# Optimization experiments

Measured on AMD Instinct MI355X. Metric: run time of the kernel, lower is better.

The kernel has to match this reference:

```python
import jax, jax.numpy as jnp
import numpy as np


def setup_inputs() -> dict:
    key = jax.random.key(0)
    ks = jax.random.split(key, 6)
    B, T, U, D_in, D_inner, V = 4, 150, 40, 512, 512, 4000
    s = 1.0 / np.sqrt(D_in)
    return {
        "enc_state": jax.random.normal(ks[0], (B, T, D_in), jnp.float32),
        "dec_state": jax.random.normal(ks[1], (B, U, D_in), jnp.float32),
        "W_enc": jax.random.normal(ks[2], (D_inner, D_in), jnp.float32) * s,
        "b_enc": jnp.zeros((D_inner,), jnp.float32),
        "W_prd": jax.random.normal(ks[3], (D_inner, D_in), jnp.float32) * s,
        "b_prd": jnp.zeros((D_inner,), jnp.float32),
        "W_proj": jax.random.normal(ks[4], (V, D_inner), jnp.float32) * (1.0 / np.sqrt(D_inner)),
        "b_proj": jnp.zeros((V,), jnp.float32),
    }


def reference(enc_state, dec_state, W_enc, b_enc, W_prd, b_prd, W_proj, b_proj):
    # pre-linear projections: [B,T,Di] and [B,U,Di]
    enc = jnp.einsum("btd,id->bti", enc_state, W_enc) + b_enc
    dec = jnp.einsum("bud,id->bui", dec_state, W_prd) + b_prd
    # broadcast add -> [B,T,U,Di] (joint_func='add', post_linear=False)
    joint = jnp.tanh(enc[:, :, None, :] + dec[:, None, :, :])
    # project to vocab and log-softmax: [B,T,U,V]
    logits = jnp.einsum("btui,vi->btuv", joint, W_proj) + b_proj
    return jax.nn.log_softmax(logits, axis=-1)
```

## Files before the change

kernel.cpp:

```cpp
#include <hip/hip_runtime.h>
#include <stdint.h>

typedef unsigned short u16;
typedef __attribute__((ext_vector_type(8))) short short8;
typedef __attribute__((ext_vector_type(4))) float floatx4;

#define D_IN  512
#define M_TOT 24000
#define M_PAD 24064
#define V_DIM 4000
#define V_PAD 4096
#define T_DIM 150
#define U_DIM 40

__device__ __forceinline__ u16 f2bf(float f) {
    union { float f; uint32_t u; } v; v.f = f;
    uint32_t r = v.u + 0x7FFF + ((v.u >> 16) & 1);
    return (u16)(r >> 16);
}

__device__ __forceinline__ void gld_lds16(const u16* g, u16* l) {
    __builtin_amdgcn_global_load_lds(
        (const __attribute__((address_space(1))) void*)g,
        (__attribute__((address_space(3))) void*)l,
        16, 0, 0);
}

__global__ void k_pre(const float* __restrict__ enc_state, const float* __restrict__ dec_state,
                      const float* __restrict__ W_enc, const float* __restrict__ b_enc,
                      const float* __restrict__ W_prd, const float* __restrict__ b_prd,
                      float* __restrict__ enc_o, float* __restrict__ dec_o,
                      float* __restrict__ sumexp)
{
    int gid = (blockIdx.y * gridDim.x + blockIdx.x) * blockDim.x + threadIdx.x;
    if (gid < M_TOT) sumexp[gid] = 0.f;

    const float* Ag; const float* Wg; const float* bg; float* Og; int M;
    int by = blockIdx.y;
    if (by < 19) { Ag = enc_state; Wg = W_enc; bg = b_enc; Og = enc_o; M = 600; }
    else         { Ag = dec_state; Wg = W_prd; bg = b_prd; Og = dec_o; M = 160; by -= 19; }

    const int row0 = by * 32;
    const int col0 = blockIdx.x * 64;
    __shared__ float Ash[32][17];
    __shared__ float Bsh[64][17];
    const int tid = threadIdx.x;
    const int tr = tid & 31;
    const int tc = tid >> 5;
    float accv[8] = {0.f,0.f,0.f,0.f,0.f,0.f,0.f,0.f};

    for (int k0 = 0; k0 < D_IN; k0 += 16) {
        __syncthreads();
        #pragma unroll
        for (int s = 0; s < 2; ++s) {
            int idx = tid + s * 256;
            int r = idx >> 4, c = idx & 15;
            Ash[r][c] = (row0 + r < M) ? Ag[(size_t)(row0 + r) * D_IN + k0 + c] : 0.f;
        }
        #pragma unroll
        for (int s = 0; s < 4; ++s) {
            int idx = tid + s * 256;
            int r = idx >> 4, c = idx & 15;
            Bsh[r][c] = Wg[(size_t)(col0 + r) * D_IN + k0 + c];
        }
        __syncthreads();
        #pragma unroll
        for (int kk = 0; kk < 16; ++kk) {
            float a = Ash[tr][kk];
            #pragma unroll
            for (int j = 0; j < 8; ++j) accv[j] += a * Bsh[tc * 8 + j][kk];
        }
    }
    if (row0 + tr < M) {
        #pragma unroll
        for (int j = 0; j < 8; ++j)
            Og[(size_t)(row0 + tr) * D_IN + col0 + tc * 8 + j] = accv[j] + bg[col0 + tc * 8 + j];
    }
}

__global__ void k_wconv(const float* __restrict__ W_proj, u16* __restrict__ Wp)
{
    int gid = blockIdx.x * blockDim.x + threadIdx.x;
    int idx2 = gid * 2;
    if (idx2 >= V_PAD * D_IN) return;
    int row = idx2 >> 9;
    ushort2 w;
    if (row < V_DIM) {
        w.x = f2bf(W_proj[idx2]);
        w.y = f2bf(W_proj[idx2 + 1]);
    } else { w.x = 0; w.y = 0; }
    *(ushort2*)&Wp[idx2] = w;
}

__global__ void k_joint(const float* __restrict__ enc_o, const float* __restrict__ dec_o,
                        u16* __restrict__ J)
{
    int m = blockIdx.x;
    int i = threadIdx.x * 2;
    ushort2 w;
    if (m < M_TOT) {
        int b = m / (T_DIM * U_DIM);
        int r = m % (T_DIM * U_DIM);
        int t = r / U_DIM, u = r % U_DIM;
        const float* e = enc_o + (size_t)(b * T_DIM + t) * D_IN + i;
        const float* d = dec_o + (size_t)(b * U_DIM + u) * D_IN + i;
        w.x = f2bf(tanhf(e[0] + d[0]));
        w.y = f2bf(tanhf(e[1] + d[1]));
    } else { w.x = 0; w.y = 0; }
    *(ushort2*)&J[(size_t)m * D_IN + i] = w;
}

__global__ __launch_bounds__(256, 2) void k_gemm(const u16* __restrict__ A,
                                                 const u16* __restrict__ Bt,
                                                 const float* __restrict__ bias,
                                                 float* __restrict__ C,
                                                 float* __restrict__ sumexp)
{
    __shared__ u16 Ash[128 * 32];
    __shared__ u16 Bsh[128 * 32];
    const int row0 = blockIdx.x * 128;
    const int col0 = blockIdx.y * 128;
    const int tid  = threadIdx.x;
    const int wave = tid >> 6;
    const int lane = tid & 63;
    const int wm = wave >> 1, wn = wave & 1;
    const int lrow = lane & 15;
    const int lq   = lane >> 4;
    const int srow = lane >> 2;
    const int scol = (lane & 3) * 8;

    floatx4 acc[4][4] = {};

    for (int k0 = 0; k0 < D_IN; k0 += 32) {
        __syncthreads();
        #pragma unroll
        for (int s = 0; s < 2; ++s) {
            int c = wave * 2 + s;
            gld_lds16(A  + (size_t)(row0 + c * 16 + srow) * D_IN + k0 + scol, &Ash[c * 16 * 32]);
            gld_lds16(Bt + (size_t)(col0 + c * 16 + srow) * D_IN + k0 + scol, &Bsh[c * 16 * 32]);
        }
        __syncthreads();
        short8 af[4], bf[4];
        #pragma unroll
        for (int mi = 0; mi < 4; ++mi)
            af[mi] = *(const short8*)&Ash[(wm * 64 + mi * 16 + lrow) * 32 + lq * 8];
        #pragma unroll
        for (int nj = 0; nj < 4; ++nj)
            bf[nj] = *(const short8*)&Bsh[(wn * 64 + nj * 16 + lrow) * 32 + lq * 8];
        #pragma unroll
        for (int mi = 0; mi < 4; ++mi)
            #pragma unroll
            for (int nj = 0; nj < 4; ++nj)
                acc[mi][nj] = __builtin_amdgcn_mfma_f32_16x16x32_bf16(af[mi], bf[nj], acc[mi][nj], 0, 0, 0);
    }

    const int cbase = col0 + wn * 64;
    const int rbase = row0 + wm * 64;
    float bv[4];
    #pragma unroll
    for (int nj = 0; nj < 4; ++nj) {
        int cc = cbase + nj * 16 + lrow;
        bv[nj] = (cc < V_DIM) ? bias[cc] : 0.f;
    }
    #pragma unroll
    for (int mi = 0; mi < 4; ++mi) {
        float se[4] = {0.f, 0.f, 0.f, 0.f};
        #pragma unroll
        for (int nj = 0; nj < 4; ++nj) {
            int cc = cbase + nj * 16 + lrow;
            bool cok = (cc < V_DIM);
            #pragma unroll
            for (int r = 0; r < 4; ++r) {
                float logit = acc[mi][nj][r] + bv[nj];
                int rr = rbase + mi * 16 + lq * 4 + r;
                if (cok) {
                    if (rr < M_TOT) C[(size_t)rr * V_DIM + cc] = logit;
                    se[r] += __expf(logit);
                }
            }
        }
        #pragma unroll
        for (int msk = 1; msk < 16; msk <<= 1) {
            #pragma unroll
            for (int r = 0; r < 4; ++r) se[r] += __shfl_xor(se[r], msk, 64);
        }
        if (lrow == 0) {
            #pragma unroll
            for (int r = 0; r < 4; ++r) {
                int rr = rbase + mi * 16 + lq * 4 + r;
                if (rr < M_TOT) atomicAdd(&sumexp[rr], se[r]);
            }
        }
    }
}

__global__ void k_lse(float* __restrict__ C, const float* __restrict__ sumexp)
{
    int gid = blockIdx.x * blockDim.x + threadIdx.x;
    if (gid >= M_TOT * (V_DIM / 4)) return;
    int row = gid / (V_DIM / 4);
    float lse = __logf(sumexp[row]);
    float4 v = *((const float4*)C + gid);
    v.x -= lse; v.y -= lse; v.z -= lse; v.w -= lse;
    *((float4*)C + gid) = v;
}

extern "C" void kernel_launch(void* const* d_in, const int* in_sizes, int n_in,
                              void* d_out, int out_size, void* d_ws, size_t ws_size,
                              hipStream_t stream)
{
    const float* enc_state = (const float*)d_in[0];
    const float* dec_state = (const float*)d_in[1];
    const float* W_enc     = (const float*)d_in[2];
    const float* b_enc     = (const float*)d_in[3];
    const float* W_prd     = (const float*)d_in[4];
    const float* b_prd     = (const float*)d_in[5];
    const float* W_proj    = (const float*)d_in[6];
    const float* b_proj    = (const float*)d_in[7];
    float* out = (float*)d_out;

    char* ws = (char*)d_ws;
    float* sumexp = (float*)(ws);
    float* enc_o  = (float*)(ws + 102400);
    float* dec_o  = (float*)(ws + 1331200);
    u16*   Wp     = (u16*)  (ws + 1658880);
    u16*   J      = (u16*)  (ws + 5853184);

    k_pre  <<<dim3(8, 24),   256, 0, stream>>>(enc_state, dec_state, W_enc, b_enc, W_prd, b_prd, enc_o, dec_o, sumexp);
    k_wconv<<<dim3(4096),    256, 0, stream>>>(W_proj, Wp);
    k_joint<<<dim3(M_PAD),   256, 0, stream>>>(enc_o, dec_o, J);
    k_gemm <<<dim3(188, 32), 256, 0, stream>>>(J, Wp, b_proj, out, sumexp);
    k_lse  <<<dim3(93750),   256, 0, stream>>>(out, sumexp);
}
```

Before: 769.5 us.

## Fuse vocab GEMM with log-softmax using full-row blocks and vectorize prep kernels

Replaces the tiled GEMM plus separate log-sum-exp pass with one kernel. Each block owns 16 full output rows, and each of its 8 waves covers 512 vocab columns. Row sum-exp is reduced in shared memory and the normalized logits are written once with nontemporal stores, which removes the atomic sumexp buffer and the extra read/write pass over the large output. The cost is that B fragments are read straight from global memory, with no LDS staging, and every block re-reads the whole bf16 projection matrix, so the kernel now leans heavily on L2/MALL bandwidth. The weight-conversion and joint kernels are also widened to 8-element vectors.

```diff
diff --git a/kernel.cpp b/kernel.cpp
--- a/kernel.cpp
+++ b/kernel.cpp
@@ -7,7 +7,6 @@
 
 #define D_IN  512
 #define M_TOT 24000
-#define M_PAD 24064
 #define V_DIM 4000
 #define V_PAD 4096
 #define T_DIM 150
@@ -19,22 +18,11 @@
     return (u16)(r >> 16);
 }
 
-__device__ __forceinline__ void gld_lds16(const u16* g, u16* l) {
-    __builtin_amdgcn_global_load_lds(
-        (const __attribute__((address_space(1))) void*)g,
-        (__attribute__((address_space(3))) void*)l,
-        16, 0, 0);
-}
-
 __global__ void k_pre(const float* __restrict__ enc_state, const float* __restrict__ dec_state,
                       const float* __restrict__ W_enc, const float* __restrict__ b_enc,
                       const float* __restrict__ W_prd, const float* __restrict__ b_prd,
-                      float* __restrict__ enc_o, float* __restrict__ dec_o,
-                      float* __restrict__ sumexp)
-{
-    int gid = (blockIdx.y * gridDim.x + blockIdx.x) * blockDim.x + threadIdx.x;
-    if (gid < M_TOT) sumexp[gid] = 0.f;
-
+                      float* __restrict__ enc_o, float* __restrict__ dec_o)
+{
     const float* Ag; const float* Wg; const float* bg; float* Og; int M;
     int by = blockIdx.y;
     if (by < 19) { Ag = enc_state; Wg = W_enc; bg = b_enc; Og = enc_o; M = 600; }
@@ -80,129 +68,135 @@
 
 __global__ void k_wconv(const float* __restrict__ W_proj, u16* __restrict__ Wp)
 {
-    int gid = blockIdx.x * blockDim.x + threadIdx.x;
-    int idx2 = gid * 2;
-    if (idx2 >= V_PAD * D_IN) return;
-    int row = idx2 >> 9;
-    ushort2 w;
+    int gid = blockIdx.x * 256 + threadIdx.x;
+    int idx8 = gid * 8;
+    int row = idx8 >> 9;
+    short8 w;
     if (row < V_DIM) {
-        w.x = f2bf(W_proj[idx2]);
-        w.y = f2bf(W_proj[idx2 + 1]);
-    } else { w.x = 0; w.y = 0; }
-    *(ushort2*)&Wp[idx2] = w;
+        const float* p = W_proj + idx8;
+        #pragma unroll
+        for (int j = 0; j < 8; ++j) w[j] = (short)f2bf(p[j]);
+    } else {
+        w = (short8){0,0,0,0,0,0,0,0};
+    }
+    *(short8*)&Wp[idx8] = w;
 }
 
 __global__ void k_joint(const float* __restrict__ enc_o, const float* __restrict__ dec_o,
                         u16* __restrict__ J)
 {
-    int m = blockIdx.x;
-    int i = threadIdx.x * 2;
-    ushort2 w;
-    if (m < M_TOT) {
-        int b = m / (T_DIM * U_DIM);
-        int r = m % (T_DIM * U_DIM);
-        int t = r / U_DIM, u = r % U_DIM;
-        const float* e = enc_o + (size_t)(b * T_DIM + t) * D_IN + i;
-        const float* d = dec_o + (size_t)(b * U_DIM + u) * D_IN + i;
-        w.x = f2bf(tanhf(e[0] + d[0]));
-        w.y = f2bf(tanhf(e[1] + d[1]));
-    } else { w.x = 0; w.y = 0; }
-    *(ushort2*)&J[(size_t)m * D_IN + i] = w;
-}
-
-__global__ __launch_bounds__(256, 2) void k_gemm(const u16* __restrict__ A,
-                                                 const u16* __restrict__ Bt,
-                                                 const float* __restrict__ bias,
-                                                 float* __restrict__ C,
-                                                 float* __restrict__ sumexp)
-{
-    __shared__ u16 Ash[128 * 32];
-    __shared__ u16 Bsh[128 * 32];
-    const int row0 = blockIdx.x * 128;
-    const int col0 = blockIdx.y * 128;
+    int m = blockIdx.x * 4 + (threadIdx.x >> 6);
+    int i = (threadIdx.x & 63) * 8;
+    int b = m / (T_DIM * U_DIM);
+    int r = m % (T_DIM * U_DIM);
+    int t = r / U_DIM, u = r % U_DIM;
+    const float4* e = (const float4*)(enc_o + (size_t)(b * T_DIM + t) * D_IN + i);
+    const float4* d = (const float4*)(dec_o + (size_t)(b * U_DIM + u) * D_IN + i);
+    float4 e0 = e[0], e1 = e[1], d0 = d[0], d1 = d[1];
+    short8 w;
+    w[0] = (short)f2bf(tanhf(e0.x + d0.x));
+    w[1] = (short)f2bf(tanhf(e0.y + d0.y));
+    w[2] = (short)f2bf(tanhf(e0.z + d0.z));
+    w[3] = (short)f2bf(tanhf(e0.w + d0.w));
+    w[4] = (short)f2bf(tanhf(e1.x + d1.x));
+    w[5] = (short)f2bf(tanhf(e1.y + d1.y));
+    w[6] = (short)f2bf(tanhf(e1.z + d1.z));
+    w[7] = (short)f2bf(tanhf(e1.w + d1.w));
+    *(short8*)&J[(size_t)m * D_IN + i] = w;
+}
+
+__global__ __launch_bounds__(512, 2) void k_fused(const u16* __restrict__ J,
+                                                  const u16* __restrict__ Bt,
+                                                  const float* __restrict__ bias,
+                                                  float* __restrict__ C)
+{
+    __shared__ u16 Alds[64 * 17 * 8];
+    __shared__ float sered[8][16];
     const int tid  = threadIdx.x;
+    const int row0 = blockIdx.x * 16;
     const int wave = tid >> 6;
     const int lane = tid & 63;
-    const int wm = wave >> 1, wn = wave & 1;
     const int lrow = lane & 15;
     const int lq   = lane >> 4;
-    const int srow = lane >> 2;
-    const int scol = (lane & 3) * 8;
-
-    floatx4 acc[4][4] = {};
-
-    for (int k0 = 0; k0 < D_IN; k0 += 32) {
-        __syncthreads();
-        #pragma unroll
-        for (int s = 0; s < 2; ++s) {
-            int c = wave * 2 + s;
-            gld_lds16(A  + (size_t)(row0 + c * 16 + srow) * D_IN + k0 + scol, &Ash[c * 16 * 32]);
-            gld_lds16(Bt + (size_t)(col0 + c * 16 + srow) * D_IN + k0 + scol, &Bsh[c * 16 * 32]);
-        }
-        __syncthreads();
-        short8 af[4], bf[4];
-        #pragma unroll
-        for (int mi = 0; mi < 4; ++mi)
-            af[mi] = *(const short8*)&Ash[(wm * 64 + mi * 16 + lrow) * 32 + lq * 8];
-        #pragma unroll
-        for (int nj = 0; nj < 4; ++nj)
-            bf[nj] = *(const short8*)&Bsh[(wn * 64 + nj * 16 + lrow) * 32 + lq * 8];
-        #pragma unroll
-        for (int mi = 0; mi < 4; ++mi)
-            #pragma unroll
-            for (int nj = 0; nj < 4; ++nj)
-                acc[mi][nj] = __builtin_amdgcn_mfma_f32_16x16x32_bf16(af[mi], bf[nj], acc[mi][nj], 0, 0, 0);
-    }
-
-    const int cbase = col0 + wn * 64;
-    const int rbase = row0 + wm * 64;
-    float bv[4];
-    #pragma unroll
-    for (int nj = 0; nj < 4; ++nj) {
-        int cc = cbase + nj * 16 + lrow;
-        bv[nj] = (cc < V_DIM) ? bias[cc] : 0.f;
-    }
-    #pragma unroll
-    for (int mi = 0; mi < 4; ++mi) {
-        float se[4] = {0.f, 0.f, 0.f, 0.f};
-        #pragma unroll
-        for (int nj = 0; nj < 4; ++nj) {
-            int cc = cbase + nj * 16 + lrow;
-            bool cok = (cc < V_DIM);
+    const int wc0  = wave << 9;
+
+    #pragma unroll
+    for (int s = 0; s < 2; ++s) {
+        int c = tid + s * 512;
+        int row = c >> 6, kch = c & 63;
+        *(short8*)&Alds[(kch * 17 + row) * 8] =
+            *(const short8*)(J + (size_t)(row0 + row) * D_IN + kch * 8);
+    }
+    __syncthreads();
+
+    floatx4 acc[32];
+    #pragma unroll
+    for (int ct = 0; ct < 32; ++ct) acc[ct] = (floatx4){0.f, 0.f, 0.f, 0.f};
+
+    const u16* bbase = Bt + (size_t)(wc0 + lrow) * D_IN + lq * 8;
+    #pragma unroll
+    for (int ct = 0; ct < 32; ++ct) {
+        if (wc0 + ct * 16 < V_DIM) {
+            const u16* bp = bbase + (size_t)ct * 16 * D_IN;
+            #pragma unroll
+            for (int kc = 0; kc < 4; ++kc) {
+                short8 afr[4], bfr[4];
+                #pragma unroll
+                for (int j = 0; j < 4; ++j) {
+                    int kk = kc * 4 + j;
+                    bfr[j] = *(const short8*)(bp + kk * 32);
+                    afr[j] = *(const short8*)&Alds[(((kk << 2) + lq) * 17 + lrow) * 8];
+                }
+                #pragma unroll
+                for (int j = 0; j < 4; ++j)
+                    acc[ct] = __builtin_amdgcn_mfma_f32_16x16x32_bf16(afr[j], bfr[j], acc[ct], 0, 0, 0);
+            }
+        }
+    }
+
+    float se[4] = {0.f, 0.f, 0.f, 0.f};
+    #pragma unroll
+    for (int ct = 0; ct < 32; ++ct) {
+        int cc = wc0 + ct * 16;
+        if (cc < V_DIM) {
+            float bv = bias[cc + lrow];
             #pragma unroll
             for (int r = 0; r < 4; ++r) {
-                float logit = acc[mi][nj][r] + bv[nj];
-                int rr = rbase + mi * 16 + lq * 4 + r;
-                if (cok) {
-                    if (rr < M_TOT) C[(size_t)rr * V_DIM + cc] = logit;
-                    se[r] += __expf(logit);
-                }
+                float lg = acc[ct][r] + bv;
+                acc[ct][r] = lg;
+                se[r] += __expf(lg);
             }
         }
-        #pragma unroll
-        for (int msk = 1; msk < 16; msk <<= 1) {
-            #pragma unroll
-            for (int r = 0; r < 4; ++r) se[r] += __shfl_xor(se[r], msk, 64);
-        }
-        if (lrow == 0) {
-            #pragma unroll
-            for (int r = 0; r < 4; ++r) {
-                int rr = rbase + mi * 16 + lq * 4 + r;
-                if (rr < M_TOT) atomicAdd(&sumexp[rr], se[r]);
-            }
-        }
-    }
-}
-
-__global__ void k_lse(float* __restrict__ C, const float* __restrict__ sumexp)
-{
-    int gid = blockIdx.x * blockDim.x + threadIdx.x;
-    if (gid >= M_TOT * (V_DIM / 4)) return;
-    int row = gid / (V_DIM / 4);
-    float lse = __logf(sumexp[row]);
-    float4 v = *((const float4*)C + gid);
-    v.x -= lse; v.y -= lse; v.z -= lse; v.w -= lse;
-    *((float4*)C + gid) = v;
+    }
+    #pragma unroll
+    for (int m = 1; m < 16; m <<= 1) {
+        #pragma unroll
+        for (int r = 0; r < 4; ++r) se[r] += __shfl_xor(se[r], m, 64);
+    }
+    if (lrow == 0) {
+        #pragma unroll
+        for (int r = 0; r < 4; ++r) sered[wave][lq * 4 + r] = se[r];
+    }
+    __syncthreads();
+    float lse[4];
+    #pragma unroll
+    for (int r = 0; r < 4; ++r) {
+        float tot = 0.f;
+        #pragma unroll
+        for (int w = 0; w < 8; ++w) tot += sered[w][lq * 4 + r];
+        lse[r] = __logf(tot);
+    }
+
+    float* crow = C + (size_t)(row0 + lq * 4) * V_DIM + lrow;
+    #pragma unroll
+    for (int ct = 0; ct < 32; ++ct) {
+        int cc = wc0 + ct * 16;
+        if (cc < V_DIM) {
+            #pragma unroll
+            for (int r = 0; r < 4; ++r)
+                __builtin_nontemporal_store(acc[ct][r] - lse[r], crow + (size_t)r * V_DIM + cc);
+        }
+    }
 }
 
 extern "C" void kernel_launch(void* const* d_in, const int* in_sizes, int n_in,
@@ -220,15 +214,13 @@
     float* out = (float*)d_out;
 
     char* ws = (char*)d_ws;
-    float* sumexp = (float*)(ws);
-    float* enc_o  = (float*)(ws + 102400);
-    float* dec_o  = (float*)(ws + 1331200);
-    u16*   Wp     = (u16*)  (ws + 1658880);
-    u16*   J      = (u16*)  (ws + 5853184);
-
-    k_pre  <<<dim3(8, 24),   256, 0, stream>>>(enc_state, dec_state, W_enc, b_enc, W_prd, b_prd, enc_o, dec_o, sumexp);
-    k_wconv<<<dim3(4096),    256, 0, stream>>>(W_proj, Wp);
-    k_joint<<<dim3(M_PAD),   256, 0, stream>>>(enc_o, dec_o, J);
-    k_gemm <<<dim3(188, 32), 256, 0, stream>>>(J, Wp, b_proj, out, sumexp);
-    k_lse  <<<dim3(93750),   256, 0, stream>>>(out, sumexp);
-}
+    float* enc_o = (float*)(ws);
+    float* dec_o = (float*)(ws + 1228800);
+    u16*   Wp    = (u16*)  (ws + 1556480);
+    u16*   J     = (u16*)  (ws + 5750784);
+
+    k_pre  <<<dim3(8, 24), 256, 0, stream>>>(enc_state, dec_state, W_enc, b_enc, W_prd, b_prd, enc_o, dec_o);
+    k_wconv<<<dim3(1024),  256, 0, stream>>>(W_proj, Wp);
+    k_joint<<<dim3(6000),  256, 0, stream>>>(enc_o, dec_o, J);
+    k_fused<<<dim3(1500),  512, 0, stream>>>(J, Wp, b_proj, out);
+}
```

Result: slower. 1.160 ms (+50.7%).
